# Performance work log

Hardware: AMD Instinct MI355X
Metric: run time of the kernel (lower is better)

The kernel has to match this reference:

```python
import jax, jax.numpy as jnp
import numpy as np
import math

HIDDEN = 1024
HEADS = 16
HEAD_DIM = HIDDEN // HEADS
B, S = 4, 2048


def setup_inputs() -> dict:
    key = jax.random.key(0)
    ks = jax.random.split(key, 9)
    std = 1.0 / math.sqrt(HIDDEN)
    return {
        "query": jax.random.normal(ks[0], (B, S, HIDDEN), jnp.float32),
        "key": jax.random.normal(ks[1], (B, S, HIDDEN), jnp.float32),
        "value": jax.random.normal(ks[2], (B, S, HIDDEN), jnp.float32),
        "q_w": jax.random.normal(ks[3], (HIDDEN, HIDDEN), jnp.float32) * std,
        "q_b": jax.random.normal(ks[4], (HIDDEN,), jnp.float32) * 0.02,
        "k_w": jax.random.normal(ks[5], (HIDDEN, HIDDEN), jnp.float32) * std,
        "k_b": jax.random.normal(ks[6], (HIDDEN,), jnp.float32) * 0.02,
        "v_w": jax.random.normal(ks[7], (HIDDEN, HIDDEN), jnp.float32) * std,
        "v_b": jax.random.normal(ks[8], (HIDDEN,), jnp.float32) * 0.02,
    }


def _split_heads(x):
    # [B, S, H] -> [B, heads, S, head_dim]
    b, s, _ = x.shape
    return x.reshape(b, s, HEADS, HEAD_DIM).transpose(0, 2, 1, 3)


def reference(query, key, value, q_w, q_b, k_w, k_b, v_w, v_b):
    # Linear projections (torch Linear: x @ W^T + b; here weights stored as [in, out])
    q = _split_heads(query @ q_w + q_b)   # [B, h, S, d]
    k = _split_heads(key @ k_w + k_b)
    v = _split_heads(value @ v_w + v_b)
    scale = 1.0 / math.sqrt(HEAD_DIM)
    scores = jnp.einsum("bhqd,bhkd->bhqk", q, k) * scale  # [B, h, S, S]
    # NOTE: faithful to source bug — context uses raw scaled scores, NOT softmax probs.
    # (softmax is computed in the original but its result is unused for the output.)
    ctx = jnp.einsum("bhqk,bhkd->bhqd", scores, v)
    ctx = ctx.transpose(0, 2, 1, 3).reshape(query.shape[0], query.shape[1], HIDDEN)
    return ctx
```

## Files before the change

### kernel.cpp

```cpp
#include <hip/hip_runtime.h>
#include <stdint.h>

#define HIDDEN 1024
#define HEADS 16
#define HEAD_DIM 64
#define BATCH 4
#define SEQ 2048
#define ROWS (BATCH * SEQ)

typedef float f32x4 __attribute__((ext_vector_type(4)));
typedef short bf16x8 __attribute__((ext_vector_type(8)));

__device__ __forceinline__ uint16_t f32_to_bf16_rne(float f) {
    uint32_t u = __float_as_uint(f);
    uint32_t r = u + 0x7FFFu + ((u >> 16) & 1u);
    return (uint16_t)(r >> 16);
}
__device__ __forceinline__ float bf16_to_f32(uint16_t u) {
    return __uint_as_float(((uint32_t)u) << 16);
}

__global__ __launch_bounds__(256) void cvt_kernel(const float* __restrict__ Xq,
                                                  const float* __restrict__ Xk,
                                                  const float* __restrict__ Xv,
                                                  uint16_t* __restrict__ Xb) {
    int z = blockIdx.x >> 13;
    const float* X = z == 0 ? Xq : (z == 1 ? Xk : Xv);
    uint16_t* out = Xb + (size_t)z * ROWS * HIDDEN;
    size_t i4 = (size_t)(blockIdx.x & 8191) * 256 + threadIdx.x;
    float4 f = ((const float4*)X)[i4];
    uint2 pk;
    pk.x = (uint32_t)f32_to_bf16_rne(f.x) | ((uint32_t)f32_to_bf16_rne(f.y) << 16);
    pk.y = (uint32_t)f32_to_bf16_rne(f.z) | ((uint32_t)f32_to_bf16_rne(f.w) << 16);
    ((uint2*)out)[i4] = pk;
}

__global__ __launch_bounds__(256) void wt_kernel(const float* __restrict__ Wk,
                                                 const float* __restrict__ Wv,
                                                 uint16_t* __restrict__ Wt) {
    const float* W = blockIdx.z == 0 ? Wk : Wv;
    uint16_t* out = Wt + (size_t)blockIdx.z * HIDDEN * HIDDEN;
    __shared__ float tile[64][65];
    int k0 = blockIdx.x * 64, n0 = blockIdx.y * 64;
    int r = threadIdx.x >> 6, c = threadIdx.x & 63;
    for (int it = 0; it < 16; ++it) {
        int rr = r + 4 * it;
        tile[rr][c] = W[(size_t)(k0 + rr) * HIDDEN + n0 + c];
    }
    __syncthreads();
    for (int it = 0; it < 16; ++it) {
        int rr = r + 4 * it;
        out[(size_t)(n0 + rr) * HIDDEN + k0 + c] = f32_to_bf16_rne(tile[c][rr]);
    }
}

__global__ __launch_bounds__(256) void proj_gemm_t(const uint16_t* __restrict__ Xkv,
                                                   const uint16_t* __restrict__ Wt,
                                                   const float* __restrict__ Bk,
                                                   const float* __restrict__ Bv,
                                                   uint16_t* __restrict__ KT) {
    const int i = blockIdx.x;
    const int xcd = i & 7;
    const int slot = i >> 3;
    const int mt = slot & 7;
    const int yhi = (slot >> 3) & 7;
    const int z = slot >> 6;
    const int yt = xcd + 8 * yhi;

    const uint16_t* A = Wt + (size_t)z * HIDDEN * HIDDEN;
    const uint16_t* B = Xkv + (size_t)z * ROWS * HIDDEN;
    const float* bias = z == 0 ? Bk : Bv;
    uint16_t* out = KT + (size_t)z * ROWS * HIDDEN;

    __shared__ uint16_t slds[16384];

    const int tid = threadIdx.x;
    const int lane = tid & 63;
    const int w = tid >> 6;
    const int wm = (w >> 1) * 64;
    const int wn = (w & 1) * 64;
    const int m_lane = lane & 15;
    const int kq = lane >> 4;
    const int m0 = mt * 128;
    const int n0 = yt * 128;

    f32x4 acc[4][4] = {};

    for (int kb = 0; kb < HIDDEN; kb += 64) {
        for (int t = 0; t < 4; ++t) {
            int gbase = (w * 4 + t) * 64;
            int g = gbase + lane;
            int r = g >> 3;
            int c = (g & 7) ^ (r & 7);
            const uint16_t* srcA = A + (size_t)(m0 + r) * HIDDEN + kb + c * 8;
            __builtin_amdgcn_global_load_lds(
                (const __attribute__((address_space(1))) uint32_t*)srcA,
                (__attribute__((address_space(3))) uint32_t*)(&slds[gbase * 8]),
                16, 0, 0);
            const uint16_t* srcB = B + (size_t)(n0 + r) * HIDDEN + kb + c * 8;
            __builtin_amdgcn_global_load_lds(
                (const __attribute__((address_space(1))) uint32_t*)srcB,
                (__attribute__((address_space(3))) uint32_t*)(&slds[8192 + gbase * 8]),
                16, 0, 0);
        }
        __syncthreads();
        for (int ks = 0; ks < 2; ++ks) {
            int cbase = ks * 4 + kq;
            bf16x8 af[4], bfr[4];
            for (int i2 = 0; i2 < 4; ++i2) {
                int r = wm + i2 * 16 + m_lane;
                int p = cbase ^ (r & 7);
                af[i2] = *(const bf16x8*)(&slds[r * 64 + p * 8]);
            }
            for (int j = 0; j < 4; ++j) {
                int nr = wn + j * 16 + m_lane;
                int p = cbase ^ (nr & 7);
                bfr[j] = *(const bf16x8*)(&slds[8192 + nr * 64 + p * 8]);
            }
            for (int i2 = 0; i2 < 4; ++i2)
                for (int j = 0; j < 4; ++j)
                    acc[i2][j] = __builtin_amdgcn_mfma_f32_16x16x32_bf16(
                        af[i2], bfr[j], acc[i2][j], 0, 0, 0);
        }
        __syncthreads();
    }

    for (int i2 = 0; i2 < 4; ++i2) {
        for (int rg = 0; rg < 4; ++rg) {
            int row = m0 + wm + i2 * 16 + kq * 4 + rg;
            float bj = bias[row];
            for (int j = 0; j < 4; ++j) {
                int col = n0 + wn + j * 16 + m_lane;
                out[(size_t)row * ROWS + col] = f32_to_bf16_rne(acc[i2][j][rg] + bj);
            }
        }
    }
}

__global__ __launch_bounds__(256) void kv_mfma(const uint16_t* __restrict__ KT,
                                               float* __restrict__ P) {
    const int bh = blockIdx.x;
    const int sc = blockIdx.y;
    const int b = bh >> 4, h = bh & 15;
    const uint16_t* Kb = KT + (size_t)(h * 64) * ROWS + (size_t)b * SEQ + sc * 256;
    const uint16_t* Vb = Kb + (size_t)HIDDEN * ROWS;

    __shared__ uint16_t slds[8192];

    const int tid = threadIdx.x;
    const int lane = tid & 63;
    const int w = tid >> 6;
    const int m_lane = lane & 15;
    const int kq = lane >> 4;

    f32x4 acc[4] = {};

    for (int kb = 0; kb < 256; kb += 64) {
        for (int t = 0; t < 2; ++t) {
            int g = t * 256 + tid;
            int r = g >> 3;
            int c = (g & 7) ^ (r & 7);
            const uint16_t* srcA = Kb + (size_t)r * ROWS + kb + c * 8;
            __builtin_amdgcn_global_load_lds(
                (const __attribute__((address_space(1))) uint32_t*)srcA,
                (__attribute__((address_space(3))) uint32_t*)(&slds[g * 8]),
                16, 0, 0);
            const uint16_t* srcB = Vb + (size_t)r * ROWS + kb + c * 8;
            __builtin_amdgcn_global_load_lds(
                (const __attribute__((address_space(1))) uint32_t*)srcB,
                (__attribute__((address_space(3))) uint32_t*)(&slds[4096 + g * 8]),
                16, 0, 0);
        }
        __syncthreads();
        for (int ks = 0; ks < 2; ++ks) {
            int cbase = ks * 4 + kq;
            int ar = w * 16 + m_lane;
            bf16x8 af = *(const bf16x8*)(&slds[ar * 64 + (cbase ^ (ar & 7)) * 8]);
            for (int j = 0; j < 4; ++j) {
                int br = j * 16 + m_lane;
                bf16x8 bf_ = *(const bf16x8*)(&slds[4096 + br * 64 + (cbase ^ (br & 7)) * 8]);
                acc[j] = __builtin_amdgcn_mfma_f32_16x16x32_bf16(af, bf_, acc[j], 0, 0, 0);
            }
        }
        __syncthreads();
    }

    float* Pp = P + ((size_t)bh * 8 + sc) * 4096;
    for (int j = 0; j < 4; ++j) {
        for (int rg = 0; rg < 4; ++rg) {
            int row = w * 16 + kq * 4 + rg;
            int col = j * 16 + m_lane;
            Pp[row * 64 + col] = acc[j][rg] * 0.125f;
        }
    }
}

__global__ __launch_bounds__(256) void wprime_kernel(const float* __restrict__ Wq,
                                                     const float* __restrict__ bq,
                                                     const float* __restrict__ P,
                                                     uint16_t* __restrict__ Wpt,
                                                     float* __restrict__ bp) {
    const int h = blockIdx.x;
    const int r0 = blockIdx.y * 64;
    const int b = blockIdx.z;
    const int tid = threadIdx.x;

    __shared__ float Mh[64][65];
    __shared__ float Wl[64][65];
    const float* Pp = P + ((size_t)(b * 16 + h)) * 8 * 4096;
    for (int it = 0; it < 16; ++it) {
        int e = it * 256 + tid;
        int a = e >> 6, c = e & 63;
        float s = 0.f;
        for (int sc = 0; sc < 8; ++sc) s += Pp[sc * 4096 + e];
        Mh[a][c] = s;
        Wl[a][c] = Wq[(size_t)(r0 + a) * HIDDEN + h * 64 + c];
    }
    __syncthreads();

    const int r = tid & 63;
    const int jbase = tid >> 6;
    float acc[16] = {};
    for (int i = 0; i < 64; ++i) {
        float wv = Wl[r][i];
        for (int jj = 0; jj < 16; ++jj)
            acc[jj] += wv * Mh[i][jbase + 4 * jj];
    }
    uint16_t* Wb = Wpt + (size_t)b * HIDDEN * HIDDEN;
    for (int jj = 0; jj < 16; ++jj) {
        int n = h * 64 + jbase + 4 * jj;
        Wb[(size_t)n * HIDDEN + r0 + r] = f32_to_bf16_rne(acc[jj]);
    }

    if (blockIdx.y == 0 && tid < 64) {
        int j = tid;
        float s = 0.f;
        for (int i = 0; i < 64; ++i) s += bq[h * 64 + i] * Mh[i][j];
        bp[b * HIDDEN + h * 64 + j] = s;
    }
}

__global__ __launch_bounds__(256) void final_gemm(const uint16_t* __restrict__ Xq,
                                                  const uint16_t* __restrict__ Wpt,
                                                  const float* __restrict__ bp,
                                                  float* __restrict__ out) {
    __shared__ uint16_t slds[16384];

    const int tid = threadIdx.x;
    const int lane = tid & 63;
    const int w = tid >> 6;
    const int wm = (w >> 1) * 64;
    const int wn = (w & 1) * 64;
    const int m_lane = lane & 15;
    const int kq = lane >> 4;
    const int m0 = blockIdx.x * 128;
    const int n0 = blockIdx.y * 128;
    const int batch = m0 >> 11;
    const uint16_t* W = Wpt + (size_t)batch * HIDDEN * HIDDEN;
    const float* bias = bp + batch * HIDDEN;

    f32x4 acc[4][4] = {};

    for (int kb = 0; kb < HIDDEN; kb += 64) {
        for (int t = 0; t < 4; ++t) {
            int gbase = (w * 4 + t) * 64;
            int g = gbase + lane;
            int r = g >> 3;
            int c = (g & 7) ^ (r & 7);
            const uint16_t* srcA = Xq + (size_t)(m0 + r) * HIDDEN + kb + c * 8;
            __builtin_amdgcn_global_load_lds(
                (const __attribute__((address_space(1))) uint32_t*)srcA,
                (__attribute__((address_space(3))) uint32_t*)(&slds[gbase * 8]),
                16, 0, 0);
            const uint16_t* srcB = W + (size_t)(n0 + r) * HIDDEN + kb + c * 8;
            __builtin_amdgcn_global_load_lds(
                (const __attribute__((address_space(1))) uint32_t*)srcB,
                (__attribute__((address_space(3))) uint32_t*)(&slds[8192 + gbase * 8]),
                16, 0, 0);
        }
        __syncthreads();
        for (int ks = 0; ks < 2; ++ks) {
            int cbase = ks * 4 + kq;
            bf16x8 af[4], bfr[4];
            for (int i = 0; i < 4; ++i) {
                int r = wm + i * 16 + m_lane;
                int p = cbase ^ (r & 7);
                af[i] = *(const bf16x8*)(&slds[r * 64 + p * 8]);
            }
            for (int j = 0; j < 4; ++j) {
                int nr = wn + j * 16 + m_lane;
                int p = cbase ^ (nr & 7);
                bfr[j] = *(const bf16x8*)(&slds[8192 + nr * 64 + p * 8]);
            }
            for (int i = 0; i < 4; ++i)
                for (int j = 0; j < 4; ++j)
                    acc[i][j] = __builtin_amdgcn_mfma_f32_16x16x32_bf16(
                        af[i], bfr[j], acc[i][j], 0, 0, 0);
        }
        __syncthreads();
    }

    for (int j = 0; j < 4; ++j) {
        int col = n0 + wn + j * 16 + m_lane;
        float bj = bias[col];
        for (int i = 0; i < 4; ++i) {
            int rbase = m0 + wm + i * 16 + kq * 4;
            for (int rg = 0; rg < 4; ++rg)
                out[(size_t)(rbase + rg) * HIDDEN + col] = acc[i][j][rg] + bj;
        }
    }
}

extern "C" void kernel_launch(void* const* d_in, const int* in_sizes, int n_in,
                              void* d_out, int out_size, void* d_ws, size_t ws_size,
                              hipStream_t stream) {
    const float* Xq = (const float*)d_in[0];
    const float* Xk = (const float*)d_in[1];
    const float* Xv = (const float*)d_in[2];
    const float* Wq = (const float*)d_in[3];
    const float* Bq = (const float*)d_in[4];
    const float* Wk = (const float*)d_in[5];
    const float* Bk = (const float*)d_in[6];
    const float* Wv = (const float*)d_in[7];
    const float* Bv = (const float*)d_in[8];
    float* out = (float*)d_out;

    char* ws = (char*)d_ws;
    uint16_t* Xb = (uint16_t*)ws;
    uint16_t* KT = (uint16_t*)(ws + 50331648);
    uint16_t* Wt = (uint16_t*)(ws + 83886080);
    float* P = (float*)(ws + 88080384);
    uint16_t* Wpt = (uint16_t*)(ws + 96468992);
    float* bp = (float*)(ws + 104857600);

    cvt_kernel<<<dim3(3 * 8192), 256, 0, stream>>>(Xq, Xk, Xv, Xb);
    wt_kernel<<<dim3(16, 16, 2), 256, 0, stream>>>(Wk, Wv, Wt);

    const uint16_t* Xkv = Xb + (size_t)ROWS * HIDDEN;
    proj_gemm_t<<<dim3(1024), 256, 0, stream>>>(Xkv, Wt, Bk, Bv, KT);
    kv_mfma<<<dim3(64, 8), 256, 0, stream>>>(KT, P);
    wprime_kernel<<<dim3(16, 16, 4), 256, 0, stream>>>(Wq, Bq, P, Wpt, bp);
    final_gemm<<<dim3(64, 8), 256, 0, stream>>>(Xb, Wpt, bp, out);
}
```

Before: 258.9 us.

## Fuse fp32-to-bf16 activation conversion into GEMM tile loads

Removes the separate conversion kernel that wrote bf16 copies of the query, key and value activations. The projection and final GEMMs now read fp32 activations directly, convert them with packed bf16 conversion instructions, and store them into the swizzled LDS tile. This avoids a full write and re-read of the bf16 activation buffers and one kernel launch. In exchange, the GEMMs read twice as many activation bytes through registers instead of direct global-to-LDS loads. Each output tile re-reads its activation rows, so the fp32 traffic is multiplied across column tiles.

```diff
diff --git a/kernel.cpp b/kernel.cpp
--- a/kernel.cpp
+++ b/kernel.cpp
@@ -19,20 +19,10 @@
 __device__ __forceinline__ float bf16_to_f32(uint16_t u) {
     return __uint_as_float(((uint32_t)u) << 16);
 }
-
-__global__ __launch_bounds__(256) void cvt_kernel(const float* __restrict__ Xq,
-                                                  const float* __restrict__ Xk,
-                                                  const float* __restrict__ Xv,
-                                                  uint16_t* __restrict__ Xb) {
-    int z = blockIdx.x >> 13;
-    const float* X = z == 0 ? Xq : (z == 1 ? Xk : Xv);
-    uint16_t* out = Xb + (size_t)z * ROWS * HIDDEN;
-    size_t i4 = (size_t)(blockIdx.x & 8191) * 256 + threadIdx.x;
-    float4 f = ((const float4*)X)[i4];
-    uint2 pk;
-    pk.x = (uint32_t)f32_to_bf16_rne(f.x) | ((uint32_t)f32_to_bf16_rne(f.y) << 16);
-    pk.y = (uint32_t)f32_to_bf16_rne(f.z) | ((uint32_t)f32_to_bf16_rne(f.w) << 16);
-    ((uint2*)out)[i4] = pk;
+__device__ __forceinline__ uint32_t cvt_pk_bf16(float lo, float hi) {
+    uint32_t r;
+    asm("v_cvt_pk_bf16_f32 %0, %1, %2" : "=v"(r) : "v"(lo), "v"(hi));
+    return r;
 }
 
 __global__ __launch_bounds__(256) void wt_kernel(const float* __restrict__ Wk,
@@ -54,7 +44,8 @@
     }
 }
 
-__global__ __launch_bounds__(256) void proj_gemm_t(const uint16_t* __restrict__ Xkv,
+__global__ __launch_bounds__(256) void proj_gemm_t(const float* __restrict__ Xk,
+                                                   const float* __restrict__ Xv,
                                                    const uint16_t* __restrict__ Wt,
                                                    const float* __restrict__ Bk,
                                                    const float* __restrict__ Bv,
@@ -68,7 +59,7 @@
     const int yt = xcd + 8 * yhi;
 
     const uint16_t* A = Wt + (size_t)z * HIDDEN * HIDDEN;
-    const uint16_t* B = Xkv + (size_t)z * ROWS * HIDDEN;
+    const float* B32 = z == 0 ? Xk : Xv;
     const float* bias = z == 0 ? Bk : Bv;
     uint16_t* out = KT + (size_t)z * ROWS * HIDDEN;
 
@@ -97,11 +88,30 @@
                 (const __attribute__((address_space(1))) uint32_t*)srcA,
                 (__attribute__((address_space(3))) uint32_t*)(&slds[gbase * 8]),
                 16, 0, 0);
-            const uint16_t* srcB = B + (size_t)(n0 + r) * HIDDEN + kb + c * 8;
-            __builtin_amdgcn_global_load_lds(
-                (const __attribute__((address_space(1))) uint32_t*)srcB,
-                (__attribute__((address_space(3))) uint32_t*)(&slds[8192 + gbase * 8]),
-                16, 0, 0);
+        }
+        for (int tp = 0; tp < 2; ++tp) {
+            float4 fa[2][2];
+            int gs[2];
+#pragma unroll
+            for (int u = 0; u < 2; ++u) {
+                int t = tp * 2 + u;
+                int g = (w * 4 + t) * 64 + lane;
+                int r = g >> 3;
+                int c = (g & 7) ^ (r & 7);
+                const float* src = B32 + (size_t)(n0 + r) * HIDDEN + kb + c * 8;
+                fa[u][0] = *(const float4*)src;
+                fa[u][1] = *(const float4*)(src + 4);
+                gs[u] = g;
+            }
+#pragma unroll
+            for (int u = 0; u < 2; ++u) {
+                uint4 pk;
+                pk.x = cvt_pk_bf16(fa[u][0].x, fa[u][0].y);
+                pk.y = cvt_pk_bf16(fa[u][0].z, fa[u][0].w);
+                pk.z = cvt_pk_bf16(fa[u][1].x, fa[u][1].y);
+                pk.w = cvt_pk_bf16(fa[u][1].z, fa[u][1].w);
+                *(uint4*)(&slds[8192 + gs[u] * 8]) = pk;
+            }
         }
         __syncthreads();
         for (int ks = 0; ks < 2; ++ks) {
@@ -240,7 +250,7 @@
     }
 }
 
-__global__ __launch_bounds__(256) void final_gemm(const uint16_t* __restrict__ Xq,
+__global__ __launch_bounds__(256) void final_gemm(const float* __restrict__ Xq,
                                                   const uint16_t* __restrict__ Wpt,
                                                   const float* __restrict__ bp,
                                                   float* __restrict__ out) {
@@ -267,16 +277,35 @@
             int g = gbase + lane;
             int r = g >> 3;
             int c = (g & 7) ^ (r & 7);
-            const uint16_t* srcA = Xq + (size_t)(m0 + r) * HIDDEN + kb + c * 8;
-            __builtin_amdgcn_global_load_lds(
-                (const __attribute__((address_space(1))) uint32_t*)srcA,
-                (__attribute__((address_space(3))) uint32_t*)(&slds[gbase * 8]),
-                16, 0, 0);
             const uint16_t* srcB = W + (size_t)(n0 + r) * HIDDEN + kb + c * 8;
             __builtin_amdgcn_global_load_lds(
                 (const __attribute__((address_space(1))) uint32_t*)srcB,
                 (__attribute__((address_space(3))) uint32_t*)(&slds[8192 + gbase * 8]),
                 16, 0, 0);
+        }
+        for (int tp = 0; tp < 2; ++tp) {
+            float4 fa[2][2];
+            int gs[2];
+#pragma unroll
+            for (int u = 0; u < 2; ++u) {
+                int t = tp * 2 + u;
+                int g = (w * 4 + t) * 64 + lane;
+                int r = g >> 3;
+                int c = (g & 7) ^ (r & 7);
+                const float* src = Xq + (size_t)(m0 + r) * HIDDEN + kb + c * 8;
+                fa[u][0] = *(const float4*)src;
+                fa[u][1] = *(const float4*)(src + 4);
+                gs[u] = g;
+            }
+#pragma unroll
+            for (int u = 0; u < 2; ++u) {
+                uint4 pk;
+                pk.x = cvt_pk_bf16(fa[u][0].x, fa[u][0].y);
+                pk.y = cvt_pk_bf16(fa[u][0].z, fa[u][0].w);
+                pk.z = cvt_pk_bf16(fa[u][1].x, fa[u][1].y);
+                pk.w = cvt_pk_bf16(fa[u][1].z, fa[u][1].w);
+                *(uint4*)(&slds[gs[u] * 8]) = pk;
+            }
         }
         __syncthreads();
         for (int ks = 0; ks < 2; ++ks) {
@@ -326,19 +355,15 @@
     float* out = (float*)d_out;
 
     char* ws = (char*)d_ws;
-    uint16_t* Xb = (uint16_t*)ws;
-    uint16_t* KT = (uint16_t*)(ws + 50331648);
-    uint16_t* Wt = (uint16_t*)(ws + 83886080);
-    float* P = (float*)(ws + 88080384);
-    uint16_t* Wpt = (uint16_t*)(ws + 96468992);
-    float* bp = (float*)(ws + 104857600);
-
-    cvt_kernel<<<dim3(3 * 8192), 256, 0, stream>>>(Xq, Xk, Xv, Xb);
+    uint16_t* KT = (uint16_t*)ws;
+    uint16_t* Wt = (uint16_t*)(ws + 33554432);
+    float* P = (float*)(ws + 37748736);
+    uint16_t* Wpt = (uint16_t*)(ws + 46137344);
+    float* bp = (float*)(ws + 54525952);
+
     wt_kernel<<<dim3(16, 16, 2), 256, 0, stream>>>(Wk, Wv, Wt);
-
-    const uint16_t* Xkv = Xb + (size_t)ROWS * HIDDEN;
-    proj_gemm_t<<<dim3(1024), 256, 0, stream>>>(Xkv, Wt, Bk, Bv, KT);
+    proj_gemm_t<<<dim3(1024), 256, 0, stream>>>(Xk, Xv, Wt, Bk, Bv, KT);
     kv_mfma<<<dim3(64, 8), 256, 0, stream>>>(KT, P);
     wprime_kernel<<<dim3(16, 16, 4), 256, 0, stream>>>(Wq, Bq, P, Wpt, bp);
-    final_gemm<<<dim3(64, 8), 256, 0, stream>>>(Xb, Wpt, bp, out);
-}
+    final_gemm<<<dim3(64, 8), 256, 0, stream>>>(Xq, Wpt, bp, out);
+}
```

Result: slower. 269.0 us (+3.9%).
